# Optimization experiments

Hardware: AMD Instinct MI355X
Metric: run time of the kernel (lower is better)

Reference implementation:

```python
import jax, jax.numpy as jnp
import numpy as np

NUM_NODES = 50000
NUM_EDGES = 1600000
NUM_GRAPHS = 64
K_HOPS = 3


def setup_inputs() -> dict:
    key = jax.random.key(0)
    ks = jax.random.split(key, 8)
    d_in, d_h, d_out = 128, 512, 16
    x = jax.random.normal(ks[0], (NUM_NODES, d_in), dtype=jnp.float32)
    edge_index = jax.random.randint(ks[1], (2, NUM_EDGES), 0, NUM_NODES, dtype=jnp.int64)
    batch = jnp.sort(jax.random.randint(ks[2], (NUM_NODES,), 0, NUM_GRAPHS, dtype=jnp.int64))
    w1 = jax.random.normal(ks[3], (d_in, d_h), dtype=jnp.float32) / np.sqrt(d_in)
    b1 = jnp.zeros((d_h,), dtype=jnp.float32)
    w2 = jax.random.normal(ks[4], (d_h, d_h), dtype=jnp.float32) / np.sqrt(d_h)
    b2 = jnp.zeros((d_h,), dtype=jnp.float32)
    wc = jax.random.normal(ks[5], (d_h, d_out), dtype=jnp.float32) / np.sqrt(d_h)
    bc = jnp.zeros((d_out,), dtype=jnp.float32)
    return {"x": x, "edge_index": edge_index, "batch": batch,
            "w1": w1, "b1": b1, "w2": w2, "b2": b2, "wc": wc, "bc": bc}


def _propagate(x, row, col, norm):
    # one hop: out[r] += x[c] * norm  (degree-normalized scatter-add)
    msg = x[col] * norm[:, None]                      # [E+N, d]
    return jax.ops.segment_sum(msg, row, num_segments=NUM_NODES)


def reference(x, edge_index, batch, w1, b1, w2, b2, wc, bc):
    # add self loops
    loops = jnp.arange(NUM_NODES, dtype=edge_index.dtype)
    row = jnp.concatenate([edge_index[0], loops])
    col = jnp.concatenate([edge_index[1], loops])
    deg = jax.ops.segment_sum(jnp.ones_like(row, dtype=jnp.float32), row,
                              num_segments=NUM_NODES)
    deg = jnp.clip(deg, 1.0)
    norm = 1.0 / deg[row]                             # [E+N]
    # K-hop propagation (eval mode: dropout / drop_node inactive)
    h = x
    for _ in range(K_HOPS):
        h = _propagate(h, row, col, norm)
    # MLP
    h = jax.nn.relu(h @ w1 + b1)
    h = h @ w2 + b2
    # global mean pool over graphs
    sums = jax.ops.segment_sum(h, batch, num_segments=NUM_GRAPHS)
    cnts = jax.ops.segment_sum(jnp.ones((h.shape[0],), dtype=h.dtype), batch,
                               num_segments=NUM_GRAPHS)
    pooled = sums / jnp.clip(cnts, 1.0)[:, None]      # [G, d_h]
    return pooled @ wc + bc                            # [G, out]
```

## Files before the change

### kernel.cpp

```cpp
#include <hip/hip_runtime.h>
#include <hip/hip_bf16.h>
#include <hip/hip_fp8.h>

#define N_NODES 50000
#define N_EDGES 1600000
#define N_GRAPHS 64
#define D_IN 128
#define D_H 512
#define D_OUT 16

#define NBUK 391
#define BUK_CAP 4608
#define P1_EDGES 4096
#define P1_BLOCKS ((N_EDGES + P1_EDGES - 1) / P1_EDGES)

typedef short bf16x8 __attribute__((ext_vector_type(8)));
typedef float f32x4 __attribute__((ext_vector_type(4)));

static __device__ __forceinline__ unsigned short f2bf(float f) {
    __hip_bfloat16 h = __float2bfloat16(f);
    return *(unsigned short*)&h;
}

static __device__ __forceinline__ float2 fp8x2_dec(unsigned short u) {
    __hip_fp8x2_e4m3 p;
    p.__x = (__hip_fp8x2_storage_t)u;
    return static_cast<float2>(p);
}

static __device__ __forceinline__ unsigned short fp8x2_enc(float a, float b) {
    __hip_fp8_e4m3 pa(a), pb(b);
    return (unsigned short)((unsigned)pa.__x | ((unsigned)pb.__x << 8));
}


__global__ __launch_bounds__(512) void partition_edges(const int* __restrict__ row,
                                                       const int* __restrict__ col,
                                                       int* __restrict__ bucket_cnt,
                                                       unsigned* __restrict__ edge_buf) {
    __shared__ unsigned recs[P1_EDGES];
    __shared__ unsigned sorted[P1_EDGES];
    __shared__ int hist4[4][NBUK];
    __shared__ int cur4[4][NBUK];
    __shared__ int gbase[NBUK];
    __shared__ int scan[512];
    int tid = threadIdx.x;
    int w2 = tid >> 7;
    int e0 = blockIdx.x * P1_EDGES;
    int m = N_EDGES - e0; if (m > P1_EDGES) m = P1_EDGES;

    for (int i = tid; i < 4 * NBUK; i += 512) ((int*)hist4)[i] = 0;
    for (int i = tid; i < 4 * NBUK; i += 512) ((int*)cur4)[i] = 0;
    __syncthreads();
    for (int i = tid; i < m; i += 512) {
        int r = row[e0 + i];
        int c = col[e0 + i];
        int buk = r >> 7;
        recs[i] = ((unsigned)buk << 23) | ((unsigned)(r & 127) << 16) | (unsigned)c;
        atomicAdd(&hist4[w2][buk], 1);
    }
    __syncthreads();
    int tot = 0;
    if (tid < NBUK) tot = hist4[0][tid] + hist4[1][tid] + hist4[2][tid] + hist4[3][tid];
    scan[tid] = (tid < NBUK) ? tot : 0;
    __syncthreads();
    for (int off = 1; off < 512; off <<= 1) {
        int v = (tid >= off) ? scan[tid - off] : 0;
        __syncthreads();
        scan[tid] += v;
        __syncthreads();
    }
    if (tid < NBUK) {
        int run = (tid == 0) ? 0 : scan[tid - 1];
        gbase[tid] = (tot > 0) ? atomicAdd(&bucket_cnt[tid], tot) : 0;
#pragma unroll
        for (int w = 0; w < 4; ++w) {
            int c = hist4[w][tid];
            hist4[w][tid] = run;
            run += c;
        }
    }
    __syncthreads();
    for (int i = tid; i < m; i += 512) {
        unsigned rec = recs[i];
        int buk = rec >> 23;
        int rank = atomicAdd(&cur4[w2][buk], 1);
        sorted[hist4[w2][buk] + rank] = rec;
    }
    __syncthreads();
    for (int p = tid; p < m; p += 512) {
        unsigned rec = sorted[p];
        int buk = rec >> 23;
        edge_buf[(size_t)buk * BUK_CAP + gbase[buk] + (p - hist4[0][buk])] = rec;
    }
}

__global__ __launch_bounds__(512) void finalize_csr(const unsigned* __restrict__ edge_buf,
                                                    const int* __restrict__ bucket_cnt,
                                                    int* __restrict__ rowptr,
                                                    float* __restrict__ invdeg,
                                                    unsigned short* __restrict__ csr_col) {
    __shared__ int hist[128], excl[128], cur[128];
    __shared__ int scan[512];
    int b = blockIdx.x;
    int tid = threadIdx.x;
    scan[tid] = (tid < NBUK) ? bucket_cnt[tid] : 0;
    __syncthreads();
    for (int off = 1; off < 512; off <<= 1) {
        int v = (tid >= off) ? scan[tid - off] : 0;
        __syncthreads();
        scan[tid] += v;
        __syncthreads();
    }
    int cnt = bucket_cnt[b];
    int base = (b == 0) ? 0 : scan[b - 1];
    const unsigned* src = edge_buf + (size_t)b * BUK_CAP;
    __syncthreads();
    if (tid < 128) { hist[tid] = 0; cur[tid] = 0; }
    __syncthreads();
    for (int i = tid; i < cnt; i += 512)
        atomicAdd(&hist[(src[i] >> 16) & 127], 1);
    __syncthreads();
    scan[tid] = (tid < 128) ? hist[tid] : 0;
    __syncthreads();
    for (int off = 1; off < 512; off <<= 1) {
        int v = (tid >= off) ? scan[tid - off] : 0;
        __syncthreads();
        scan[tid] += v;
        __syncthreads();
    }
    if (tid < 128) excl[tid] = (tid == 0) ? 0 : scan[tid - 1];
    __syncthreads();
    int r = b * 128 + tid;
    if (tid < 128 && r < N_NODES) {
        rowptr[r] = base + excl[tid];
        invdeg[r] = 1.0f / (float)(hist[tid] + 1);
    }
    if (b == NBUK - 1 && tid == 0) rowptr[N_NODES] = base + cnt;
    for (int i = tid; i < cnt; i += 512) {
        unsigned rec = src[i];
        int rl = (rec >> 16) & 127;
        int pos = excl[rl] + atomicAdd(&cur[rl], 1);
        csr_col[base + pos] = (unsigned short)(rec & 0xFFFFu);
    }
}


__global__ __launch_bounds__(256) void prep(const float* __restrict__ x,
                                            unsigned short* __restrict__ xf,
                                            const float* __restrict__ w1,
                                            unsigned short* __restrict__ w1p,
                                            const float* __restrict__ w2,
                                            const float* __restrict__ wc,
                                            const float* __restrict__ b2,
                                            const float* __restrict__ bc,
                                            const int* __restrict__ batch,
                                            float* __restrict__ wcomb,
                                            float* __restrict__ bcomb,
                                            int* __restrict__ gcnt) {
    int b = blockIdx.x;
    int tid = threadIdx.x;
    if (b < 12500) {
        int i = b * 256 + tid;
        float2 v = ((const float2*)x)[i];
        xf[i] = fp8x2_enc(v.x, v.y);
        return;
    }
    if (b < 12756) {
        int i = (b - 12500) * 256 + tid;
        int j = i & 7, lane = (i >> 3) & 63, s = (i >> 9) & 3, t = i >> 11;
        int k = s * 32 + (lane >> 4) * 8 + j;
        int n = t * 16 + (lane & 15);
        w1p[i] = f2bf(w1[(size_t)k * D_H + n]);
        return;
    }
    int fb = b - 12756;
    if (fb == 33) {
        if (tid < N_GRAPHS) {
            int g = tid;
            int lo = 0, hi = N_NODES;
            while (lo < hi) { int mid = (lo + hi) >> 1; if (batch[mid] < g) lo = mid + 1; else hi = mid; }
            int a = lo;
            lo = 0; hi = N_NODES;
            while (lo < hi) { int mid = (lo + hi) >> 1; if (batch[mid] < g + 1) lo = mid + 1; else hi = mid; }
            gcnt[g] = lo - a;
        }
        return;
    }
    int o = tid & 15, kl = tid >> 4;
    int k = fb * 16 + kl;
    if (k > D_H) return;
    const float* wr = (k < D_H) ? (w2 + (size_t)k * D_H) : b2;
    float s = 0.f;
    for (int j = 0; j < D_H; j += 4) {
        s += wr[j + 0] * wc[(j + 0) * D_OUT + o]
           + wr[j + 1] * wc[(j + 1) * D_OUT + o]
           + wr[j + 2] * wc[(j + 2) * D_OUT + o]
           + wr[j + 3] * wc[(j + 3) * D_OUT + o];
    }
    if (k < D_H) wcomb[k * D_OUT + o] = s;
    else         bcomb[o] = s + bc[o];
}


__global__ __launch_bounds__(128) void propagate_fp8(const unsigned short* __restrict__ xin,
                                                     unsigned short* __restrict__ out8,
                                                     unsigned* __restrict__ out16,
                                                     int last, float extra,
                                                     const int* __restrict__ rowptr,
                                                     const unsigned short* __restrict__ csr_col,
                                                     const float* __restrict__ invdeg) {
    int wave = threadIdx.x >> 6;
    int lane = threadIdx.x & 63;
    int r = blockIdx.x * 2 + wave;
    if (r >= N_NODES) return;
    int beg = rowptr[r], end = rowptr[r + 1];
    float2 sv = fp8x2_dec(xin[(size_t)r * 64 + lane]);
    float acc0 = sv.x, acc1 = sv.y;
    for (int cs = beg; cs < end; cs += 64) {
        int nn = end - cs; if (nn > 64) nn = 64;
        int colv = (int)csr_col[cs + (lane < nn ? lane : 0)];
        int j = 0;
        for (; j + 16 <= nn; j += 16) {
            unsigned short uu[16];
#pragma unroll
            for (int q = 0; q < 16; ++q) {
                int c = __shfl(colv, j + q, 64);
                uu[q] = xin[(size_t)c * 64 + lane];
            }
#pragma unroll
            for (int q = 0; q < 16; ++q) {
                float2 v = fp8x2_dec(uu[q]);
                acc0 += v.x; acc1 += v.y;
            }
        }
        for (; j + 4 <= nn; j += 4) {
            unsigned short u0, u1, u2, u3;
            {
                int c0 = __shfl(colv, j + 0, 64), c1 = __shfl(colv, j + 1, 64);
                int c2 = __shfl(colv, j + 2, 64), c3 = __shfl(colv, j + 3, 64);
                u0 = xin[(size_t)c0 * 64 + lane];
                u1 = xin[(size_t)c1 * 64 + lane];
                u2 = xin[(size_t)c2 * 64 + lane];
                u3 = xin[(size_t)c3 * 64 + lane];
            }
            float2 v0 = fp8x2_dec(u0), v1 = fp8x2_dec(u1);
            float2 v2 = fp8x2_dec(u2), v3 = fp8x2_dec(u3);
            acc0 += v0.x + v1.x + v2.x + v3.x;
            acc1 += v0.y + v1.y + v2.y + v3.y;
        }
        for (; j < nn; ++j) {
            int c = __shfl(colv, j, 64);
            float2 v = fp8x2_dec(xin[(size_t)c * 64 + lane]);
            acc0 += v.x; acc1 += v.y;
        }
    }
    float s = invdeg[r] * extra;
    acc0 *= s; acc1 *= s;
    if (last) {
        out16[(size_t)r * 64 + lane] = (unsigned)f2bf(acc0) | ((unsigned)f2bf(acc1) << 16);
    } else {
        out8[(size_t)r * 64 + lane] = fp8x2_enc(acc0, acc1);
    }
}


__global__ __launch_bounds__(256) void gemm_mfma_pool(const unsigned short* __restrict__ h3b,
                                                      const unsigned short* __restrict__ w1p,
                                                      const float* __restrict__ b1,
                                                      const int* __restrict__ batch,
                                                      float* __restrict__ gsum) {
    __shared__ float hls[64][132];
    __shared__ int bls[64];
    int tid = threadIdx.x;
    int lane = tid & 63, wave = tid >> 6;
    int quad = lane >> 4, l15 = lane & 15;
    int mbase = blockIdx.x * 64;
    int nbase = blockIdx.y * 128;

    int m = mbase + wave * 16 + l15;
    int mc = m < N_NODES ? m : N_NODES - 1;
    const unsigned short* arow = h3b + (size_t)mc * 128 + quad * 8;
    bf16x8 afrag[4];
#pragma unroll
    for (int s = 0; s < 4; ++s)
        afrag[s] = *(const bf16x8*)(arow + s * 32);

    f32x4 acc[8];
#pragma unroll
    for (int t = 0; t < 8; ++t) acc[t] = (f32x4){0.f, 0.f, 0.f, 0.f};

    const unsigned short* bbase = w1p + ((size_t)(blockIdx.y * 8) * 4 * 64 + lane) * 8;
#pragma unroll
    for (int t = 0; t < 8; ++t) {
#pragma unroll
        for (int s = 0; s < 4; ++s) {
            bf16x8 bfrag = *(const bf16x8*)(bbase + (size_t)(t * 4 + s) * 64 * 8);
            acc[t] = __builtin_amdgcn_mfma_f32_16x16x32_bf16(afrag[s], bfrag, acc[t], 0, 0, 0);
        }
    }

    if (tid < 64) {
        int mm = mbase + tid;
        bls[tid] = (mm < N_NODES) ? batch[mm] : 0;
    }
#pragma unroll
    for (int t = 0; t < 8; ++t)
#pragma unroll
        for (int rg = 0; rg < 4; ++rg)
            hls[wave * 16 + quad * 4 + rg][t * 16 + l15] = acc[t][rg];
    __syncthreads();

    int c = tid & 127, half = tid >> 7;
    float bias = b1[nbase + c];
    int r0 = half * 32;
    int cur = bls[r0];
    float s = 0.f;
    for (int r = r0; r < r0 + 32; ++r) {
        int mm = mbase + r;
        if (mm >= N_NODES) break;
        int g = bls[r];
        float v = hls[r][c] + bias;
        v = v > 0.f ? v : 0.f;
        if (g != cur) { atomicAdd(&gsum[cur * D_H + nbase + c], s); s = 0.f; cur = g; }
        s += v;
    }
    atomicAdd(&gsum[cur * D_H + nbase + c], s);
}


__global__ __launch_bounds__(256) void final_pool(const float* __restrict__ gsum,
                                                  const int* __restrict__ gcnt,
                                                  const float* __restrict__ wcomb,
                                                  const float* __restrict__ bcomb,
                                                  float* __restrict__ out) {
    int g = blockIdx.x;
    int tid = threadIdx.x;
    __shared__ float p[D_H];
    __shared__ float part[16][17];
    int c = gcnt[g]; if (c < 1) c = 1;
    float inv = 1.0f / (float)c;
    p[tid] = gsum[g * D_H + tid] * inv;
    p[tid + 256] = gsum[g * D_H + tid + 256] * inv;
    __syncthreads();
    int o = tid & 15, ch = tid >> 4;
    int k0 = ch * 32;
    float s = 0.f;
    for (int k = k0; k < k0 + 32; ++k)
        s += p[k] * wcomb[k * D_OUT + o];
    part[ch][o] = s;
    __syncthreads();
    if (tid < D_OUT) {
        float t = bcomb[tid];
        for (int ch2 = 0; ch2 < 16; ++ch2) t += part[ch2][tid];
        out[g * D_OUT + tid] = t;
    }
}


extern "C" void kernel_launch(void* const* d_in, const int* in_sizes, int n_in,
                              void* d_out, int out_size, void* d_ws, size_t ws_size,
                              hipStream_t stream) {
    const float* x     = (const float*)d_in[0];
    const int*   eidx  = (const int*)d_in[1];
    const int*   batch = (const int*)d_in[2];
    const float* w1    = (const float*)d_in[3];
    const float* b1    = (const float*)d_in[4];
    const float* w2    = (const float*)d_in[5];
    const float* b2    = (const float*)d_in[6];
    const float* wc    = (const float*)d_in[7];
    const float* bc    = (const float*)d_in[8];
    float* out = (float*)d_out;
    const int* row = eidx;
    const int* col = eidx + N_EDGES;

    char* p = (char*)d_ws;
    auto alloc = [&](size_t bytes) { char* q = p; p += (bytes + 255) & ~(size_t)255; return q; };
    char* zbase = p;
    int*   bucket_cnt = (int*)alloc((size_t)NBUK * 4);
    float* gsum       = (float*)alloc((size_t)N_GRAPHS * D_H * 4);
    size_t zbytes = (size_t)(p - zbase);
    int*   rowptr  = (int*)alloc((size_t)(N_NODES + 1) * 4);
    int*   gcnt    = (int*)alloc((size_t)N_GRAPHS * 4);
    float* invdeg  = (float*)alloc((size_t)N_NODES * 4);
    float* wcomb   = (float*)alloc((size_t)D_H * D_OUT * 4);
    float* bcomb   = (float*)alloc((size_t)D_OUT * 4);
    unsigned* edge_buf = (unsigned*)alloc((size_t)NBUK * BUK_CAP * 4);
    unsigned short* csr_col = (unsigned short*)alloc((size_t)N_EDGES * 2);
    unsigned short* xf  = (unsigned short*)alloc((size_t)N_NODES * 64 * 2);
    unsigned short* h0f = (unsigned short*)alloc((size_t)N_NODES * 64 * 2);
    unsigned short* h1f = (unsigned short*)alloc((size_t)N_NODES * 64 * 2);
    unsigned* h3b  = (unsigned*)alloc((size_t)N_NODES * 64 * 4);
    unsigned short* w1p = (unsigned short*)alloc((size_t)D_IN * D_H * 2);

    (void)hipMemsetAsync(zbase, 0, zbytes, stream);

    prep<<<12790, 256, 0, stream>>>(x, xf, w1, w1p, w2, wc, b2, bc, batch,
                                    wcomb, bcomb, gcnt);

    partition_edges<<<P1_BLOCKS, 512, 0, stream>>>(row, col, bucket_cnt, edge_buf);
    finalize_csr<<<NBUK, 512, 0, stream>>>(edge_buf, bucket_cnt, rowptr, invdeg, csr_col);

    int pgrid = (N_NODES + 1) / 2;
    propagate_fp8<<<pgrid, 128, 0, stream>>>(xf,  h0f, nullptr, 0, 8.0f,
                                             rowptr, csr_col, invdeg);
    propagate_fp8<<<pgrid, 128, 0, stream>>>(h0f, h1f, nullptr, 0, 8.0f,
                                             rowptr, csr_col, invdeg);
    propagate_fp8<<<pgrid, 128, 0, stream>>>(h1f, nullptr, h3b, 1, 1.0f / 64.0f,
                                             rowptr, csr_col, invdeg);

    dim3 ggrid((N_NODES + 63) / 64, D_H / 128);
    gemm_mfma_pool<<<ggrid, 256, 0, stream>>>((const unsigned short*)h3b, w1p, b1, batch, gsum);
    final_pool<<<N_GRAPHS, 256, 0, stream>>>(gsum, gcnt, wcomb, bcomb, out);
}
```

Before: 266.8 us.

## Assign one block per graph in GEMM+pool to remove global atomics

Measured after the change: 263.7 us. Within noise of the previous version (-1.2%).

```diff
diff --git a/kernel.cpp b/kernel.cpp
--- a/kernel.cpp
+++ b/kernel.cpp
@@ -157,7 +157,8 @@
                                             const int* __restrict__ batch,
                                             float* __restrict__ wcomb,
                                             float* __restrict__ bcomb,
-                                            int* __restrict__ gcnt) {
+                                            int* __restrict__ gcnt,
+                                            int* __restrict__ gstart) {
     int b = blockIdx.x;
     int tid = threadIdx.x;
     if (b < 12500) {
@@ -184,6 +185,8 @@
             lo = 0; hi = N_NODES;
             while (lo < hi) { int mid = (lo + hi) >> 1; if (batch[mid] < g + 1) lo = mid + 1; else hi = mid; }
             gcnt[g] = lo - a;
+            gstart[g] = a;
+            if (g == N_GRAPHS - 1) gstart[N_GRAPHS] = N_NODES;
         }
         return;
     }
@@ -265,67 +268,68 @@
 }
 
 
-__global__ __launch_bounds__(256) void gemm_mfma_pool(const unsigned short* __restrict__ h3b,
-                                                      const unsigned short* __restrict__ w1p,
-                                                      const float* __restrict__ b1,
-                                                      const int* __restrict__ batch,
-                                                      float* __restrict__ gsum) {
+__global__ __launch_bounds__(256) void gemm_graph_pool(const unsigned short* __restrict__ h3b,
+                                                       const unsigned short* __restrict__ w1p,
+                                                       const float* __restrict__ b1,
+                                                       const int* __restrict__ gstart,
+                                                       float* __restrict__ gsum) {
     __shared__ float hls[64][132];
-    __shared__ int bls[64];
+    __shared__ float sum2[2][128];
     int tid = threadIdx.x;
     int lane = tid & 63, wave = tid >> 6;
     int quad = lane >> 4, l15 = lane & 15;
-    int mbase = blockIdx.x * 64;
+    int g = blockIdx.x;
     int nbase = blockIdx.y * 128;
-
-    int m = mbase + wave * 16 + l15;
-    int mc = m < N_NODES ? m : N_NODES - 1;
-    const unsigned short* arow = h3b + (size_t)mc * 128 + quad * 8;
-    bf16x8 afrag[4];
-#pragma unroll
-    for (int s = 0; s < 4; ++s)
-        afrag[s] = *(const bf16x8*)(arow + s * 32);
-
-    f32x4 acc[8];
-#pragma unroll
-    for (int t = 0; t < 8; ++t) acc[t] = (f32x4){0.f, 0.f, 0.f, 0.f};
-
+    int r0 = gstart[g], r1 = gstart[g + 1];
+
+    bf16x8 bfr[32];
     const unsigned short* bbase = w1p + ((size_t)(blockIdx.y * 8) * 4 * 64 + lane) * 8;
 #pragma unroll
-    for (int t = 0; t < 8; ++t) {
-#pragma unroll
-        for (int s = 0; s < 4; ++s) {
-            bf16x8 bfrag = *(const bf16x8*)(bbase + (size_t)(t * 4 + s) * 64 * 8);
-            acc[t] = __builtin_amdgcn_mfma_f32_16x16x32_bf16(afrag[s], bfrag, acc[t], 0, 0, 0);
-        }
-    }
-
-    if (tid < 64) {
-        int mm = mbase + tid;
-        bls[tid] = (mm < N_NODES) ? batch[mm] : 0;
-    }
-#pragma unroll
-    for (int t = 0; t < 8; ++t)
-#pragma unroll
-        for (int rg = 0; rg < 4; ++rg)
-            hls[wave * 16 + quad * 4 + rg][t * 16 + l15] = acc[t][rg];
-    __syncthreads();
+    for (int i = 0; i < 32; ++i)
+        bfr[i] = *(const bf16x8*)(bbase + (size_t)i * 64 * 8);
 
     int c = tid & 127, half = tid >> 7;
     float bias = b1[nbase + c];
-    int r0 = half * 32;
-    int cur = bls[r0];
-    float s = 0.f;
-    for (int r = r0; r < r0 + 32; ++r) {
-        int mm = mbase + r;
-        if (mm >= N_NODES) break;
-        int g = bls[r];
-        float v = hls[r][c] + bias;
-        v = v > 0.f ? v : 0.f;
-        if (g != cur) { atomicAdd(&gsum[cur * D_H + nbase + c], s); s = 0.f; cur = g; }
-        s += v;
-    }
-    atomicAdd(&gsum[cur * D_H + nbase + c], s);
+    float gacc = 0.f;
+
+    for (int mbase = r0; mbase < r1; mbase += 64) {
+        int m = mbase + wave * 16 + l15;
+        int mc = m < N_NODES ? m : N_NODES - 1;
+        const unsigned short* arow = h3b + (size_t)mc * 128 + quad * 8;
+        bf16x8 afrag[4];
+#pragma unroll
+        for (int s = 0; s < 4; ++s)
+            afrag[s] = *(const bf16x8*)(arow + s * 32);
+
+        f32x4 acc[8];
+#pragma unroll
+        for (int t = 0; t < 8; ++t) acc[t] = (f32x4){0.f, 0.f, 0.f, 0.f};
+#pragma unroll
+        for (int t = 0; t < 8; ++t)
+#pragma unroll
+            for (int s = 0; s < 4; ++s)
+                acc[t] = __builtin_amdgcn_mfma_f32_16x16x32_bf16(afrag[s], bfr[t * 4 + s],
+                                                                 acc[t], 0, 0, 0);
+        __syncthreads();
+#pragma unroll
+        for (int t = 0; t < 8; ++t)
+#pragma unroll
+            for (int rg = 0; rg < 4; ++rg)
+                hls[wave * 16 + quad * 4 + rg][t * 16 + l15] = acc[t][rg];
+        __syncthreads();
+
+        int rend = r1 - mbase; if (rend > 64) rend = 64;
+        int rs = half * 32;
+        int re = rs + 32 < rend ? rs + 32 : rend;
+        for (int r = rs; r < re; ++r) {
+            float v = hls[r][c] + bias;
+            gacc += v > 0.f ? v : 0.f;
+        }
+    }
+    sum2[half][c] = gacc;
+    __syncthreads();
+    if (half == 0)
+        gsum[g * D_H + nbase + c] = sum2[0][c] + sum2[1][c];
 }
 
 
@@ -378,10 +382,11 @@
     auto alloc = [&](size_t bytes) { char* q = p; p += (bytes + 255) & ~(size_t)255; return q; };
     char* zbase = p;
     int*   bucket_cnt = (int*)alloc((size_t)NBUK * 4);
-    float* gsum       = (float*)alloc((size_t)N_GRAPHS * D_H * 4);
     size_t zbytes = (size_t)(p - zbase);
+    float* gsum    = (float*)alloc((size_t)N_GRAPHS * D_H * 4);
     int*   rowptr  = (int*)alloc((size_t)(N_NODES + 1) * 4);
     int*   gcnt    = (int*)alloc((size_t)N_GRAPHS * 4);
+    int*   gstart  = (int*)alloc((size_t)(N_GRAPHS + 1) * 4);
     float* invdeg  = (float*)alloc((size_t)N_NODES * 4);
     float* wcomb   = (float*)alloc((size_t)D_H * D_OUT * 4);
     float* bcomb   = (float*)alloc((size_t)D_OUT * 4);
@@ -396,7 +401,7 @@
     (void)hipMemsetAsync(zbase, 0, zbytes, stream);
 
     prep<<<12790, 256, 0, stream>>>(x, xf, w1, w1p, w2, wc, b2, bc, batch,
-                                    wcomb, bcomb, gcnt);
+                                    wcomb, bcomb, gcnt, gstart);
 
     partition_edges<<<P1_BLOCKS, 512, 0, stream>>>(row, col, bucket_cnt, edge_buf);
     finalize_csr<<<NBUK, 512, 0, stream>>>(edge_buf, bucket_cnt, rowptr, invdeg, csr_col);
@@ -409,7 +414,8 @@
     propagate_fp8<<<pgrid, 128, 0, stream>>>(h1f, nullptr, h3b, 1, 1.0f / 64.0f,
                                              rowptr, csr_col, invdeg);
 
-    dim3 ggrid((N_NODES + 63) / 64, D_H / 128);
-    gemm_mfma_pool<<<ggrid, 256, 0, stream>>>((const unsigned short*)h3b, w1p, b1, batch, gsum);
+    dim3 ggrid(N_GRAPHS, D_H / 128);
+    gemm_graph_pool<<<ggrid, 256, 0, stream>>>((const unsigned short*)h3b, w1p, b1,
+                                               gstart, gsum);
     final_pool<<<N_GRAPHS, 256, 0, stream>>>(gsum, gcnt, wcomb, bcomb, out);
 }
```
